# Kernel optimization log

Hardware: AMD Instinct MI355X
Metric: run time of the kernel (lower is better)

The kernel has to match this reference:

```python
import jax, jax.numpy as jnp
import numpy as np

B, N, DIMS, F_DIMS = 4, 16384, 3, 64


def setup_inputs() -> dict:
    key = jax.random.key(0)
    k1, k2, k3 = jax.random.split(key, 3)
    pc = jax.random.normal(k1, (B, N, DIMS), dtype=jnp.float32)
    feats = jax.random.normal(k2, (B, N, F_DIMS), dtype=jnp.float32)
    # single random permutation shared across the batch (tf.random.shuffle(tf.range(N)))
    perm = jax.random.permutation(k3, N).astype(jnp.int32)
    return {"pc": pc, "feats": feats, "perm": perm}


def reference(pc, feats, perm):
    """Faithful JAX port of RandomSample.call.

    pc:    (B, N, dims)   spatial coords
    feats: (B, N, f_dims) features
    perm:  (N,)           random permutation of range(N)
    """
    n = pc.shape[1]
    m = n // 2  # body hardcodes N // 2 regardless of self.scale
    valid_idx = perm[:m]
    invalid_idx = perm[m:]

    valid_pc = jnp.take(pc, valid_idx, axis=1)        # (B, M, dims)
    valid_feats = jnp.take(feats, valid_idx, axis=1)  # (B, M, f_dims)
    invalid_pc = jnp.take(pc, invalid_idx, axis=1)    # (B, M, dims)

    # brute-force KNN: squared euclidean distance of invalid queries vs valid points
    q2 = jnp.sum(invalid_pc * invalid_pc, axis=-1, keepdims=True)   # (B, M, 1)
    p2 = jnp.sum(valid_pc * valid_pc, axis=-1)[:, None, :]          # (B, 1, M)
    cross = jnp.einsum('bqd,bpd->bqp', invalid_pc, valid_pc)        # (B, M, M)
    d2 = q2 - 2.0 * cross + p2                                      # (B, M, M)

    # K=2 nearest; keep the 2nd neighbour index, as in n_idx = knn(...)[:, :, 1]
    _, knn_idx = jax.lax.top_k(-d2, 2)                              # (B, M, 2)
    n_idx = knn_idx[:, :, 1].astype(jnp.int32)                      # (B, M)

    rnds = perm[None, :]  # (1, N), matches tf.expand_dims(shuffle, 0)
    return valid_pc, valid_feats, n_idx, rnds
```

## Files before the change

### kernel.cpp

```cpp
#include <hip/hip_runtime.h>

#define BB 4
#define NN 16384
#define MM 8192
#define FD 64
#define CHUNK 256
#define QPT 2
#define TPB 256
#define QPB (TPB * QPT)

#define OUT0 0
#define OUT1 98304
#define OUT2 2195456
#define OUT3 2228224

#define CAND_BYTES ((size_t)BB * MM * 16)

struct Partial { double m1, m2; };

__device__ __forceinline__ float sumsq3_rn(float x, float y, float z) {
  return __fadd_rn(__fadd_rn(__fmul_rn(x, x), __fmul_rn(y, y)), __fmul_rn(z, z));
}

__device__ __forceinline__ double mkkey(float d2, int k) {
  return __hiloint2double(__float_as_int(d2), k);
}
#define KEY_INIT __hiloint2double(0x7F800000, 0x7FFFFFFF)

__global__ __launch_bounds__(256) void gather_kernel(
    const float* __restrict__ pc, const float* __restrict__ feats,
    const int* __restrict__ perm, float* __restrict__ out,
    float4* __restrict__ cand) {
  int idx = blockIdx.x * 256 + threadIdx.x;
  const int F4_TOT = BB * MM * FD / 4;
  const int PTS    = BB * MM;
  if (idx < F4_TOT) {
    int f4 = idx & 15;
    int r  = (idx >> 4) & (MM - 1);
    int b  = idx >> 17;
    int vi = perm[r];
    const float4* src = (const float4*)(feats + ((b * NN + vi) << 6));
    float4* dst = (float4*)(out + OUT1) + idx;
    *dst = src[f4];
  } else if (idx < F4_TOT + PTS) {
    int k = idx - F4_TOT;
    int r = k & (MM - 1);
    int b = k >> 13;
    int vi = perm[r];
    const float* src = pc + (b * NN + vi) * 3;
    float px = src[0], py = src[1], pz = src[2];
    float* dst = out + OUT0 + k * 3;
    dst[0] = px; dst[1] = py; dst[2] = pz;
    cand[k] = make_float4(px + px, py + py, pz + pz, sumsq3_rn(px, py, pz));
  } else if (idx < F4_TOT + PTS + NN) {
    int k = idx - F4_TOT - PTS;
    out[OUT3 + k] = (float)perm[k];
  }
}

__global__ __launch_bounds__(256) void knn_kernel(
    const float* __restrict__ pc, const int* __restrict__ perm,
    const float4* __restrict__ cand,
    Partial* __restrict__ part, float* __restrict__ out, int nchunk) {
  #pragma clang fp contract(off)
  int blk = blockIdx.x;
  int c  = blk % nchunk;
  int qb = blk / nchunk;
  int q0 = qb * QPB + threadIdx.x;
  int b  = qb >> 4;

  float qx[QPT], qy[QPT], qz[QPT], q2[QPT];
  double m1[QPT], m2[QPT];
  #pragma unroll
  for (int s = 0; s < QPT; ++s) {
    int q = q0 + s * TPB;
    int j = q & (MM - 1);
    int qi = perm[MM + j];
    const float* qp = pc + (b * NN + qi) * 3;
    qx[s] = qp[0]; qy[s] = qp[1]; qz[s] = qp[2];
    q2[s] = sumsq3_rn(qx[s], qy[s], qz[s]);
    m1[s] = KEY_INIT; m2[s] = KEY_INIT;
  }

  __shared__ float4 tile[CHUNK];

  int span = MM / nchunk;
  int begin = c * span, end = begin + span;

  for (int t0 = begin; t0 < end; t0 += CHUNK) {
    __syncthreads();
    tile[threadIdx.x] = cand[b * MM + t0 + threadIdx.x];
    __syncthreads();
    #pragma unroll 8
    for (int k = 0; k < CHUNK; ++k) {
      float4 t = tile[k];
      int idx = t0 + k;
      #pragma unroll
      for (int s = 0; s < QPT; ++s) {
        float cross2 = __fmaf_rn(qz[s], t.z,
                       __fmaf_rn(qy[s], t.y, __fmul_rn(qx[s], t.x)));
        float d2 = __fadd_rn(__fsub_rn(q2[s], cross2), t.w);
        double key = mkkey(d2, idx);
        m2[s] = fmin(fmax(key, m1[s]), m2[s]);
        m1[s] = fmin(key, m1[s]);
      }
    }
  }

  #pragma unroll
  for (int s = 0; s < QPT; ++s) {
    int q = q0 + s * TPB;
    if (part != nullptr) {
      Partial pr; pr.m1 = m1[s]; pr.m2 = m2[s];
      part[q * nchunk + c] = pr;
    } else {
      out[OUT2 + q] = (float)__double2loint(m2[s]);
    }
  }
}

__global__ __launch_bounds__(256) void knn_merge_kernel(
    const Partial* __restrict__ part, float* __restrict__ out, int nchunk) {
  int q = blockIdx.x * 256 + threadIdx.x;
  double m1 = KEY_INIT, m2 = KEY_INIT;
  for (int c = 0; c < nchunk; ++c) {
    Partial p = part[q * nchunk + c];
    m2 = fmin(fmax(p.m1, m1), m2);
    m1 = fmin(p.m1, m1);
    m2 = fmin(fmax(p.m2, m1), m2);
    m1 = fmin(p.m2, m1);
  }
  out[OUT2 + q] = (float)__double2loint(m2);
}

extern "C" void kernel_launch(void* const* d_in, const int* in_sizes, int n_in,
                              void* d_out, int out_size, void* d_ws, size_t ws_size,
                              hipStream_t stream) {
  const float* pc    = (const float*)d_in[0];
  const float* feats = (const float*)d_in[1];
  const int*   perm  = (const int*)d_in[2];
  float* out = (float*)d_out;

  float4* cand = (float4*)d_ws;
  char*   rest = (char*)d_ws + CAND_BYTES;
  size_t  avail = ws_size > CAND_BYTES ? ws_size - CAND_BYTES : 0;

  gather_kernel<<<2240, 256, 0, stream>>>(pc, feats, perm, out, cand);

  int nchunk = 1;
  if      (avail >= (size_t)BB * MM * 32 * sizeof(Partial)) nchunk = 32;
  else if (avail >= (size_t)BB * MM * 16 * sizeof(Partial)) nchunk = 16;
  else if (avail >= (size_t)BB * MM * 8  * sizeof(Partial)) nchunk = 8;
  else if (avail >= (size_t)BB * MM * 4  * sizeof(Partial)) nchunk = 4;
  else if (avail >= (size_t)BB * MM * 2  * sizeof(Partial)) nchunk = 2;

  int qblocks = BB * MM / QPB;
  if (nchunk > 1) {
    Partial* part = (Partial*)rest;
    knn_kernel<<<qblocks * nchunk, TPB, 0, stream>>>(pc, perm, cand, part, out, nchunk);
    knn_merge_kernel<<<BB * MM / 256, 256, 0, stream>>>(part, out, nchunk);
  } else {
    knn_kernel<<<qblocks, TPB, 0, stream>>>(pc, perm, cand, nullptr, out, 1);
  }
}
```

Before: 75.63 us.

## Prune KNN key updates using a precomputed second-nearest distance bound

Adds a bound kernel that computes, for each query, the second-smallest squared distance over the first 512 candidates. The main KNN loop compares each fp32 distance to this bound and only builds the packed double key and runs the min/max updates when a distance could enter the top-2. This removes most of the double-precision fmin/fmax work per candidate in exchange for an extra small kernel, a per-candidate compare and branch, and possible wave divergence.

```diff
diff --git a/kernel.cpp b/kernel.cpp
--- a/kernel.cpp
+++ b/kernel.cpp
@@ -8,18 +8,25 @@
 #define QPT 2
 #define TPB 256
 #define QPB (TPB * QPT)
+#define NBOUND 512
 
 #define OUT0 0
 #define OUT1 98304
 #define OUT2 2195456
 #define OUT3 2228224
 
-#define CAND_BYTES ((size_t)BB * MM * 16)
+#define CAND_BYTES  ((size_t)BB * MM * 16)
+#define BOUND_BYTES ((size_t)BB * MM * 4)
 
 struct Partial { double m1, m2; };
 
 __device__ __forceinline__ float sumsq3_rn(float x, float y, float z) {
   return __fadd_rn(__fadd_rn(__fmul_rn(x, x), __fmul_rn(y, y)), __fmul_rn(z, z));
+}
+__device__ __forceinline__ float dist2_rn(float qx, float qy, float qz, float q2,
+                                          float4 t) {
+  float cross2 = __fmaf_rn(qz, t.z, __fmaf_rn(qy, t.y, __fmul_rn(qx, t.x)));
+  return __fadd_rn(__fsub_rn(q2, cross2), t.w);
 }
 
 __device__ __forceinline__ double mkkey(float d2, int k) {
@@ -58,9 +65,31 @@
   }
 }
 
+__global__ __launch_bounds__(256) void bound_kernel(
+    const float* __restrict__ pc, const int* __restrict__ perm,
+    const float4* __restrict__ cand, float* __restrict__ bound2) {
+  #pragma clang fp contract(off)
+  int q = blockIdx.x * 256 + threadIdx.x;
+  int b = q >> 13;
+  int j = q & (MM - 1);
+  int qi = perm[MM + j];
+  const float* qp = pc + (b * NN + qi) * 3;
+  float qx = qp[0], qy = qp[1], qz = qp[2];
+  float q2 = sumsq3_rn(qx, qy, qz);
+  float m1 = 3.4e38f, m2 = 3.4e38f;
+  const float4* cb = cand + b * MM;
+  #pragma unroll 8
+  for (int k = 0; k < NBOUND; ++k) {
+    float d2 = dist2_rn(qx, qy, qz, q2, cb[k]);
+    m2 = __builtin_amdgcn_fmed3f(d2, m1, m2);
+    m1 = fminf(d2, m1);
+  }
+  bound2[q] = m2;
+}
+
 __global__ __launch_bounds__(256) void knn_kernel(
     const float* __restrict__ pc, const int* __restrict__ perm,
-    const float4* __restrict__ cand,
+    const float4* __restrict__ cand, const float* __restrict__ bound2,
     Partial* __restrict__ part, float* __restrict__ out, int nchunk) {
   #pragma clang fp contract(off)
   int blk = blockIdx.x;
@@ -69,7 +98,7 @@
   int q0 = qb * QPB + threadIdx.x;
   int b  = qb >> 4;
 
-  float qx[QPT], qy[QPT], qz[QPT], q2[QPT];
+  float qx[QPT], qy[QPT], qz[QPT], q2[QPT], bf[QPT];
   double m1[QPT], m2[QPT];
   #pragma unroll
   for (int s = 0; s < QPT; ++s) {
@@ -79,6 +108,7 @@
     const float* qp = pc + (b * NN + qi) * 3;
     qx[s] = qp[0]; qy[s] = qp[1]; qz[s] = qp[2];
     q2[s] = sumsq3_rn(qx[s], qy[s], qz[s]);
+    bf[s] = bound2[q];
     m1[s] = KEY_INIT; m2[s] = KEY_INIT;
   }
 
@@ -91,18 +121,19 @@
     __syncthreads();
     tile[threadIdx.x] = cand[b * MM + t0 + threadIdx.x];
     __syncthreads();
-    #pragma unroll 8
+    #pragma unroll 4
     for (int k = 0; k < CHUNK; ++k) {
       float4 t = tile[k];
       int idx = t0 + k;
-      #pragma unroll
-      for (int s = 0; s < QPT; ++s) {
-        float cross2 = __fmaf_rn(qz[s], t.z,
-                       __fmaf_rn(qy[s], t.y, __fmul_rn(qx[s], t.x)));
-        float d2 = __fadd_rn(__fsub_rn(q2[s], cross2), t.w);
-        double key = mkkey(d2, idx);
-        m2[s] = fmin(fmax(key, m1[s]), m2[s]);
-        m1[s] = fmin(key, m1[s]);
+      float d2a = dist2_rn(qx[0], qy[0], qz[0], q2[0], t);
+      float d2b = dist2_rn(qx[1], qy[1], qz[1], q2[1], t);
+      if (__builtin_expect((d2a <= bf[0]) | (d2b <= bf[1]), 0)) {
+        double ka = mkkey(d2a, idx);
+        double kb = mkkey(d2b, idx);
+        m2[0] = fmin(fmax(ka, m1[0]), m2[0]);
+        m1[0] = fmin(ka, m1[0]);
+        m2[1] = fmin(fmax(kb, m1[1]), m2[1]);
+        m1[1] = fmin(kb, m1[1]);
       }
     }
   }
@@ -141,11 +172,15 @@
   const int*   perm  = (const int*)d_in[2];
   float* out = (float*)d_out;
 
-  float4* cand = (float4*)d_ws;
-  char*   rest = (char*)d_ws + CAND_BYTES;
-  size_t  avail = ws_size > CAND_BYTES ? ws_size - CAND_BYTES : 0;
+  float4* cand   = (float4*)d_ws;
+  float*  bound2 = (float*)((char*)d_ws + CAND_BYTES);
+  char*   rest   = (char*)d_ws + CAND_BYTES + BOUND_BYTES;
+  size_t  used   = CAND_BYTES + BOUND_BYTES;
+  size_t  avail  = ws_size > used ? ws_size - used : 0;
 
   gather_kernel<<<2240, 256, 0, stream>>>(pc, feats, perm, out, cand);
+
+  bound_kernel<<<BB * MM / 256, 256, 0, stream>>>(pc, perm, cand, bound2);
 
   int nchunk = 1;
   if      (avail >= (size_t)BB * MM * 32 * sizeof(Partial)) nchunk = 32;
@@ -157,9 +192,11 @@
   int qblocks = BB * MM / QPB;
   if (nchunk > 1) {
     Partial* part = (Partial*)rest;
-    knn_kernel<<<qblocks * nchunk, TPB, 0, stream>>>(pc, perm, cand, part, out, nchunk);
+    knn_kernel<<<qblocks * nchunk, TPB, 0, stream>>>(pc, perm, cand, bound2,
+                                                     part, out, nchunk);
     knn_merge_kernel<<<BB * MM / 256, 256, 0, stream>>>(part, out, nchunk);
   } else {
-    knn_kernel<<<qblocks, TPB, 0, stream>>>(pc, perm, cand, nullptr, out, 1);
-  }
-}
+    knn_kernel<<<qblocks, TPB, 0, stream>>>(pc, perm, cand, bound2,
+                                            nullptr, out, 1);
+  }
+}
```

New measurement: 109.7 us. +45.1%, slower.

## Prune brute-force KNN via x-coordinate binning and per-query distance bounds

Applied to the files above, without the earlier changes.

Sorts candidate points and queries into 128 bins by x coordinate using histogram, prefix-sum and scatter kernels. A bound kernel computes each query's 2nd-nearest distance over the first 1024 candidates. Each KNN block then scans only the sorted candidate range whose x lies within that bound of its queries. This cuts the full M×M distance scan but adds several small kernels, atomics and a memset, and tie-breaking on equal distances depends on the stored original indices. The META_BYTES macro has an unbalanced parenthesis but is never used, and the bins assume coordinates roughly within ±6.

```diff
diff --git a/kernel.cpp b/kernel.cpp
--- a/kernel.cpp
+++ b/kernel.cpp
@@ -8,24 +8,45 @@
 #define QPT 2
 #define TPB 256
 #define QPB (TPB * QPT)
+#define NBOUND 1024
+#define BINS 128
 
 #define OUT0 0
 #define OUT1 98304
 #define OUT2 2195456
 #define OUT3 2228224
 
+#define CAND_OFF   0
 #define CAND_BYTES ((size_t)BB * MM * 16)
+#define SCAND_OFF  (CAND_OFF + CAND_BYTES)
+#define BOUND_OFF  (SCAND_OFF + CAND_BYTES)
+#define BOUND_BYTES ((size_t)BB * MM * 4)
+#define SKIDX_OFF  (BOUND_OFF + BOUND_BYTES)
+#define SQID_OFF   (SKIDX_OFF + BOUND_BYTES)
+#define META_OFF   (SQID_OFF + BOUND_BYTES)
+#define META_BYTES ((size_t)16384
+#define FIXED_BYTES (META_OFF + 16384)
 
 struct Partial { double m1, m2; };
 
 __device__ __forceinline__ float sumsq3_rn(float x, float y, float z) {
   return __fadd_rn(__fadd_rn(__fmul_rn(x, x), __fmul_rn(y, y)), __fmul_rn(z, z));
 }
-
+__device__ __forceinline__ float dist2_rn(float qx, float qy, float qz, float q2,
+                                          float4 t) {
+  float cross2 = __fmaf_rn(qz, t.z, __fmaf_rn(qy, t.y, __fmul_rn(qx, t.x)));
+  return __fadd_rn(__fsub_rn(q2, cross2), t.w);
+}
 __device__ __forceinline__ double mkkey(float d2, int k) {
   return __hiloint2double(__float_as_int(d2), k);
 }
 #define KEY_INIT __hiloint2double(0x7F800000, 0x7FFFFFFF)
+
+__device__ __forceinline__ int bin128(float v2x) {
+  float f = floorf((v2x + 12.0f) * (BINS / 24.0f));
+  f = fmaxf(0.0f, fminf((float)(BINS - 1), f));
+  return (int)f;
+}
 
 __global__ __launch_bounds__(256) void gather_kernel(
     const float* __restrict__ pc, const float* __restrict__ feats,
@@ -58,49 +79,168 @@
   }
 }
 
+__global__ __launch_bounds__(256) void hist_kernel(
+    const float* __restrict__ pc, const int* __restrict__ perm,
+    const float4* __restrict__ cand, int* __restrict__ meta) {
+  int idx = blockIdx.x * 256 + threadIdx.x;
+  if (idx < BB * MM) {
+    int b = idx >> 13;
+    atomicAdd(&meta[0 + b * BINS + bin128(cand[idx].x)], 1);
+  } else if (idx < 2 * BB * MM) {
+    int qid = idx - BB * MM;
+    int b = qid >> 13, j = qid & (MM - 1);
+    int qi = perm[MM + j];
+    float qx = pc[(b * NN + qi) * 3];
+    atomicAdd(&meta[512 + b * BINS + bin128(qx + qx)], 1);
+  }
+}
+
+__global__ void prefix_kernel(int* __restrict__ meta) {
+  int t = threadIdx.x;
+  if (t < 4) {
+    const int* h = meta + 0 + t * BINS;
+    int* o = meta + 2048 + t * 129;
+    int acc = 0;
+    for (int i = 0; i < BINS; ++i) { o[i] = acc; acc += h[i]; }
+    o[BINS] = acc;
+  } else if (t < 8) {
+    int b = t - 4;
+    const int* h = meta + 512 + b * BINS;
+    int* o = meta + 2564 + b * 129;
+    int acc = 0;
+    for (int i = 0; i < BINS; ++i) { o[i] = acc; acc += h[i]; }
+    o[BINS] = acc;
+  }
+}
+
+__global__ __launch_bounds__(256) void scatter_kernel(
+    const float* __restrict__ pc, const int* __restrict__ perm,
+    const float4* __restrict__ cand, int* __restrict__ meta,
+    float4* __restrict__ scand, int* __restrict__ skidx,
+    int* __restrict__ sqid) {
+  int idx = blockIdx.x * 256 + threadIdx.x;
+  if (idx < BB * MM) {
+    int b = idx >> 13;
+    float4 cv = cand[idx];
+    int bin = bin128(cv.x);
+    int pos = meta[2048 + b * 129 + bin] + atomicAdd(&meta[1024 + b * BINS + bin], 1);
+    int g = (b << 13) + pos;
+    scand[g] = cv;
+    skidx[g] = idx & (MM - 1);
+  } else if (idx < 2 * BB * MM) {
+    int qid = idx - BB * MM;
+    int b = qid >> 13, j = qid & (MM - 1);
+    int qi = perm[MM + j];
+    float qx = pc[(b * NN + qi) * 3];
+    int bin = bin128(qx + qx);
+    int pos = meta[2564 + b * 129 + bin] + atomicAdd(&meta[1536 + b * BINS + bin], 1);
+    sqid[(b << 13) + pos] = j;
+  }
+}
+
+__global__ __launch_bounds__(256) void bound_kernel(
+    const float* __restrict__ pc, const int* __restrict__ perm,
+    const float4* __restrict__ cand, float* __restrict__ bound2) {
+  #pragma clang fp contract(off)
+  int gid = blockIdx.x * 256 + threadIdx.x;
+  int q = gid >> 3, t = gid & 7;
+  int b = q >> 13, j = q & (MM - 1);
+  int qi = perm[MM + j];
+  const float* qp = pc + (b * NN + qi) * 3;
+  float qx = qp[0], qy = qp[1], qz = qp[2];
+  float q2 = sumsq3_rn(qx, qy, qz);
+  float m1 = 3.4e38f, m2 = 3.4e38f;
+  const float4* cb = cand + (b << 13) + t * (NBOUND / 8);
+  #pragma unroll 4
+  for (int i = 0; i < NBOUND / 8; ++i) {
+    float d2 = dist2_rn(qx, qy, qz, q2, cb[i]);
+    m2 = __builtin_amdgcn_fmed3f(d2, m1, m2);
+    m1 = fminf(d2, m1);
+  }
+  #pragma unroll
+  for (int mask = 1; mask < 8; mask <<= 1) {
+    float o1 = __shfl_xor(m1, mask);
+    float o2 = __shfl_xor(m2, mask);
+    float n1 = fminf(m1, o1);
+    float n2 = fminf(fmaxf(m1, o1), fminf(m2, o2));
+    m1 = n1; m2 = n2;
+  }
+  if (t == 0) bound2[q] = m2;
+}
+
 __global__ __launch_bounds__(256) void knn_kernel(
     const float* __restrict__ pc, const int* __restrict__ perm,
-    const float4* __restrict__ cand,
+    const float4* __restrict__ scand, const int* __restrict__ skidx,
+    const int* __restrict__ sqid, const float* __restrict__ bound2,
+    const int* __restrict__ meta,
     Partial* __restrict__ part, float* __restrict__ out, int nchunk) {
   #pragma clang fp contract(off)
-  int blk = blockIdx.x;
-  int c  = blk % nchunk;
-  int qb = blk / nchunk;
-  int q0 = qb * QPB + threadIdx.x;
+  int c  = blockIdx.x % nchunk;
+  int qb = blockIdx.x / nchunk;
   int b  = qb >> 4;
+  int bbase = b << 13;
+  int tid = threadIdx.x;
 
   float qx[QPT], qy[QPT], qz[QPT], q2[QPT];
-  double m1[QPT], m2[QPT];
+  int qorig[QPT];
+  float myLo = 3.4e38f, myHi = -3.4e38f;
   #pragma unroll
   for (int s = 0; s < QPT; ++s) {
-    int q = q0 + s * TPB;
-    int j = q & (MM - 1);
+    int slot = (qb & 15) * QPB + tid + s * TPB;
+    int j = sqid[bbase + slot];
+    qorig[s] = bbase + j;
     int qi = perm[MM + j];
     const float* qp = pc + (b * NN + qi) * 3;
     qx[s] = qp[0]; qy[s] = qp[1]; qz[s] = qp[2];
     q2[s] = sumsq3_rn(qx[s], qy[s], qz[s]);
-    m1[s] = KEY_INIT; m2[s] = KEY_INIT;
-  }
+    float bf = bound2[bbase + j];
+    float r2 = 2.0f * sqrtf(bf + 1e-3f) * 1.0001f;
+    myLo = fminf(myLo, (qx[s] + qx[s]) - r2);
+    myHi = fmaxf(myHi, (qx[s] + qx[s]) + r2);
+  }
+
+  __shared__ float rlo[256], rhi[256];
+  rlo[tid] = myLo; rhi[tid] = myHi;
+  __syncthreads();
+  for (int s2 = 128; s2 > 0; s2 >>= 1) {
+    if (tid < s2) {
+      rlo[tid] = fminf(rlo[tid], rlo[tid + s2]);
+      rhi[tid] = fmaxf(rhi[tid], rhi[tid + s2]);
+    }
+    __syncthreads();
+  }
+  float wlo = rlo[0], whi = rhi[0];
+
+  const int* koff = meta + 2048 + b * 129;
+  int blo = bin128(wlo), bhi = bin128(whi);
+  int plo = bbase + koff[blo];
+  int phi = bbase + koff[bhi + 1];
+  int len = phi - plo;
+  int chunklen = (len + nchunk - 1) / nchunk;
+  int start = plo + c * chunklen;
+  int end = min(start + chunklen, phi);
+
+  double m1[QPT] = {KEY_INIT, KEY_INIT};
+  double m2[QPT] = {KEY_INIT, KEY_INIT};
 
   __shared__ float4 tile[CHUNK];
-
-  int span = MM / nchunk;
-  int begin = c * span, end = begin + span;
-
-  for (int t0 = begin; t0 < end; t0 += CHUNK) {
+  __shared__ int   tidxs[CHUNK];
+
+  for (int t0 = start; t0 < end; t0 += CHUNK) {
     __syncthreads();
-    tile[threadIdx.x] = cand[b * MM + t0 + threadIdx.x];
+    int pos = min(t0 + tid, phi - 1);
+    tile[tid]  = scand[pos];
+    tidxs[tid] = skidx[pos];
     __syncthreads();
-    #pragma unroll 8
-    for (int k = 0; k < CHUNK; ++k) {
+    int kmax = min(CHUNK, end - t0);
+    #pragma unroll 4
+    for (int k = 0; k < kmax; ++k) {
       float4 t = tile[k];
-      int idx = t0 + k;
+      int ki = tidxs[k];
       #pragma unroll
       for (int s = 0; s < QPT; ++s) {
-        float cross2 = __fmaf_rn(qz[s], t.z,
-                       __fmaf_rn(qy[s], t.y, __fmul_rn(qx[s], t.x)));
-        float d2 = __fadd_rn(__fsub_rn(q2[s], cross2), t.w);
-        double key = mkkey(d2, idx);
+        float d2 = dist2_rn(qx[s], qy[s], qz[s], q2[s], t);
+        double key = mkkey(d2, ki);
         m2[s] = fmin(fmax(key, m1[s]), m2[s]);
         m1[s] = fmin(key, m1[s]);
       }
@@ -109,12 +249,11 @@
 
   #pragma unroll
   for (int s = 0; s < QPT; ++s) {
-    int q = q0 + s * TPB;
     if (part != nullptr) {
       Partial pr; pr.m1 = m1[s]; pr.m2 = m2[s];
-      part[q * nchunk + c] = pr;
+      part[qorig[s] * nchunk + c] = pr;
     } else {
-      out[OUT2 + q] = (float)__double2loint(m2[s]);
+      out[OUT2 + qorig[s]] = (float)__double2loint(m2[s]);
     }
   }
 }
@@ -141,11 +280,23 @@
   const int*   perm  = (const int*)d_in[2];
   float* out = (float*)d_out;
 
-  float4* cand = (float4*)d_ws;
-  char*   rest = (char*)d_ws + CAND_BYTES;
-  size_t  avail = ws_size > CAND_BYTES ? ws_size - CAND_BYTES : 0;
+  char* ws = (char*)d_ws;
+  float4* cand   = (float4*)(ws + CAND_OFF);
+  float4* scand  = (float4*)(ws + SCAND_OFF);
+  float*  bound2 = (float*)(ws + BOUND_OFF);
+  int*    skidx  = (int*)(ws + SKIDX_OFF);
+  int*    sqid   = (int*)(ws + SQID_OFF);
+  int*    meta   = (int*)(ws + META_OFF);
+  char*   rest   = ws + FIXED_BYTES;
+  size_t  avail  = ws_size > FIXED_BYTES ? ws_size - FIXED_BYTES : 0;
+
+  hipMemsetAsync(meta, 0, 2048 * sizeof(int), stream);
 
   gather_kernel<<<2240, 256, 0, stream>>>(pc, feats, perm, out, cand);
+  hist_kernel<<<256, 256, 0, stream>>>(pc, perm, cand, meta);
+  prefix_kernel<<<1, 256, 0, stream>>>(meta);
+  scatter_kernel<<<256, 256, 0, stream>>>(pc, perm, cand, meta, scand, skidx, sqid);
+  bound_kernel<<<1024, 256, 0, stream>>>(pc, perm, cand, bound2);
 
   int nchunk = 1;
   if      (avail >= (size_t)BB * MM * 32 * sizeof(Partial)) nchunk = 32;
@@ -157,9 +308,11 @@
   int qblocks = BB * MM / QPB;
   if (nchunk > 1) {
     Partial* part = (Partial*)rest;
-    knn_kernel<<<qblocks * nchunk, TPB, 0, stream>>>(pc, perm, cand, part, out, nchunk);
+    knn_kernel<<<qblocks * nchunk, TPB, 0, stream>>>(pc, perm, scand, skidx, sqid,
+                                                     bound2, meta, part, out, nchunk);
     knn_merge_kernel<<<BB * MM / 256, 256, 0, stream>>>(part, out, nchunk);
   } else {
-    knn_kernel<<<qblocks, TPB, 0, stream>>>(pc, perm, cand, nullptr, out, 1);
-  }
-}
+    knn_kernel<<<qblocks, TPB, 0, stream>>>(pc, perm, scand, skidx, sqid,
+                                            bound2, meta, nullptr, out, 1);
+  }
+}
```

Measured after the change: 194.6 us. 2.57x slower.

## Split KNN into float value scan, chunk merge, and index recovery pass

Applied to the files above, without the earlier changes.

The main scan now tracks only the two smallest float distances per query with fmed3/fmin. It drops the packed double keys that carried the index, which cuts the inner loop to cheap 32-bit ops. A merge kernel finds which chunks hold the top two values, and a recovery kernel rescans only those chunks per query with wavefront-parallel double-key reduction to recover the exact index and tie-breaking. This adds two kernel launches and extra workspace, and the fallback nchunk is now fixed at 8 even if the workspace is smaller.

```diff
diff --git a/kernel.cpp b/kernel.cpp
--- a/kernel.cpp
+++ b/kernel.cpp
@@ -5,23 +5,28 @@
 #define MM 8192
 #define FD 64
 #define CHUNK 256
-#define QPT 2
 #define TPB 256
-#define QPB (TPB * QPT)
+#define QPB 512
 
 #define OUT0 0
 #define OUT1 98304
 #define OUT2 2195456
 #define OUT3 2228224
 
+#define CAND_OFF   0
 #define CAND_BYTES ((size_t)BB * MM * 16)
-
-struct Partial { double m1, m2; };
+#define CPAIR_OFF  (CAND_OFF + CAND_BYTES)
+#define CPAIR_BYTES ((size_t)BB * MM * 8)
+#define PART_OFF   (CPAIR_OFF + CPAIR_BYTES)
 
 __device__ __forceinline__ float sumsq3_rn(float x, float y, float z) {
   return __fadd_rn(__fadd_rn(__fmul_rn(x, x), __fmul_rn(y, y)), __fmul_rn(z, z));
 }
-
+__device__ __forceinline__ float dist2_rn(float qx, float qy, float qz, float q2,
+                                          float4 t) {
+  float cross2 = __fmaf_rn(qz, t.z, __fmaf_rn(qy, t.y, __fmul_rn(qx, t.x)));
+  return __fadd_rn(__fsub_rn(q2, cross2), t.w);
+}
 __device__ __forceinline__ double mkkey(float d2, int k) {
   return __hiloint2double(__float_as_int(d2), k);
 }
@@ -58,28 +63,25 @@
   }
 }
 
-__global__ __launch_bounds__(256) void knn_kernel(
+__global__ __launch_bounds__(256) void knn_val_kernel(
     const float* __restrict__ pc, const int* __restrict__ perm,
-    const float4* __restrict__ cand,
-    Partial* __restrict__ part, float* __restrict__ out, int nchunk) {
+    const float4* __restrict__ cand, float2* __restrict__ part, int nchunk) {
   #pragma clang fp contract(off)
-  int blk = blockIdx.x;
-  int c  = blk % nchunk;
-  int qb = blk / nchunk;
+  int c  = blockIdx.x % nchunk;
+  int qb = blockIdx.x / nchunk;
   int q0 = qb * QPB + threadIdx.x;
   int b  = qb >> 4;
 
-  float qx[QPT], qy[QPT], qz[QPT], q2[QPT];
-  double m1[QPT], m2[QPT];
+  float qx[2], qy[2], qz[2], q2[2], m1[2], m2[2];
   #pragma unroll
-  for (int s = 0; s < QPT; ++s) {
+  for (int s = 0; s < 2; ++s) {
     int q = q0 + s * TPB;
     int j = q & (MM - 1);
     int qi = perm[MM + j];
     const float* qp = pc + (b * NN + qi) * 3;
     qx[s] = qp[0]; qy[s] = qp[1]; qz[s] = qp[2];
     q2[s] = sumsq3_rn(qx[s], qy[s], qz[s]);
-    m1[s] = KEY_INIT; m2[s] = KEY_INIT;
+    m1[s] = 3.4e38f; m2[s] = 3.4e38f;
   }
 
   __shared__ float4 tile[CHUNK];
@@ -94,43 +96,77 @@
     #pragma unroll 8
     for (int k = 0; k < CHUNK; ++k) {
       float4 t = tile[k];
-      int idx = t0 + k;
       #pragma unroll
-      for (int s = 0; s < QPT; ++s) {
-        float cross2 = __fmaf_rn(qz[s], t.z,
-                       __fmaf_rn(qy[s], t.y, __fmul_rn(qx[s], t.x)));
-        float d2 = __fadd_rn(__fsub_rn(q2[s], cross2), t.w);
-        double key = mkkey(d2, idx);
-        m2[s] = fmin(fmax(key, m1[s]), m2[s]);
-        m1[s] = fmin(key, m1[s]);
+      for (int s = 0; s < 2; ++s) {
+        float d2 = dist2_rn(qx[s], qy[s], qz[s], q2[s], t);
+        m2[s] = __builtin_amdgcn_fmed3f(d2, m1[s], m2[s]);
+        m1[s] = fminf(d2, m1[s]);
       }
     }
   }
 
   #pragma unroll
-  for (int s = 0; s < QPT; ++s) {
+  for (int s = 0; s < 2; ++s) {
     int q = q0 + s * TPB;
-    if (part != nullptr) {
-      Partial pr; pr.m1 = m1[s]; pr.m2 = m2[s];
-      part[q * nchunk + c] = pr;
-    } else {
-      out[OUT2 + q] = (float)__double2loint(m2[s]);
-    }
+    part[q * nchunk + c] = make_float2(m1[s], m2[s]);
   }
 }
 
-__global__ __launch_bounds__(256) void knn_merge_kernel(
-    const Partial* __restrict__ part, float* __restrict__ out, int nchunk) {
+__global__ __launch_bounds__(256) void merge_kernel(
+    const float2* __restrict__ part, int2* __restrict__ cpair, int nchunk) {
   int q = blockIdx.x * 256 + threadIdx.x;
+  double k1 = KEY_INIT, k2 = KEY_INIT;
+  for (int c = 0; c < nchunk; ++c) {
+    float2 p = part[q * nchunk + c];
+    double a = mkkey(p.x, c);
+    double d = mkkey(p.y, c);
+    k2 = fmin(fmax(a, k1), k2);
+    k1 = fmin(a, k1);
+    k2 = fmin(fmax(d, k1), k2);
+    k1 = fmin(d, k1);
+  }
+  cpair[q] = make_int2(__double2loint(k1), __double2loint(k2));
+}
+
+__global__ __launch_bounds__(256) void recover_kernel(
+    const float* __restrict__ pc, const int* __restrict__ perm,
+    const float4* __restrict__ cand, const int2* __restrict__ cpair,
+    float* __restrict__ out, int nchunk) {
+  #pragma clang fp contract(off)
+  int wid = threadIdx.x >> 6, lane = threadIdx.x & 63;
+  int q = blockIdx.x * 4 + wid;
+  int b = q >> 13, j = q & (MM - 1);
+  int qi = perm[MM + j];
+  const float* qp = pc + (b * NN + qi) * 3;
+  float qx = qp[0], qy = qp[1], qz = qp[2];
+  float q2 = sumsq3_rn(qx, qy, qz);
+  int2 cp = cpair[q];
+  int clen = MM / nchunk;
+  const float4* cb = cand + (b << 13);
+
   double m1 = KEY_INIT, m2 = KEY_INIT;
-  for (int c = 0; c < nchunk; ++c) {
-    Partial p = part[q * nchunk + c];
-    m2 = fmin(fmax(p.m1, m1), m2);
-    m1 = fmin(p.m1, m1);
-    m2 = fmin(fmax(p.m2, m1), m2);
-    m1 = fmin(p.m2, m1);
+  #pragma unroll
+  for (int pass = 0; pass < 2; ++pass) {
+    int c = pass == 0 ? cp.x : cp.y;
+    if (pass == 1 && cp.y == cp.x) break;
+    int base = c * clen;
+    for (int i = lane; i < clen; i += 64) {
+      float4 t = cb[base + i];
+      float d2 = dist2_rn(qx, qy, qz, q2, t);
+      double key = mkkey(d2, base + i);
+      m2 = fmin(fmax(key, m1), m2);
+      m1 = fmin(key, m1);
+    }
   }
-  out[OUT2 + q] = (float)__double2loint(m2);
+  #pragma unroll
+  for (int mask = 1; mask < 64; mask <<= 1) {
+    double o1 = __shfl_xor(m1, mask);
+    double o2 = __shfl_xor(m2, mask);
+    double n1 = fmin(m1, o1);
+    double n2 = fmin(fmax(m1, o1), fmin(m2, o2));
+    m1 = n1; m2 = n2;
+  }
+  if (lane == 0) out[OUT2 + q] = (float)__double2loint(m2);
 }
 
 extern "C" void kernel_launch(void* const* d_in, const int* in_sizes, int n_in,
@@ -141,25 +177,19 @@
   const int*   perm  = (const int*)d_in[2];
   float* out = (float*)d_out;
 
-  float4* cand = (float4*)d_ws;
-  char*   rest = (char*)d_ws + CAND_BYTES;
-  size_t  avail = ws_size > CAND_BYTES ? ws_size - CAND_BYTES : 0;
+  char* ws = (char*)d_ws;
+  float4* cand  = (float4*)(ws + CAND_OFF);
+  int2*   cpair = (int2*)(ws + CPAIR_OFF);
+  float2* part  = (float2*)(ws + PART_OFF);
+  size_t  avail = ws_size > PART_OFF ? ws_size - PART_OFF : 0;
 
   gather_kernel<<<2240, 256, 0, stream>>>(pc, feats, perm, out, cand);
 
-  int nchunk = 1;
-  if      (avail >= (size_t)BB * MM * 32 * sizeof(Partial)) nchunk = 32;
-  else if (avail >= (size_t)BB * MM * 16 * sizeof(Partial)) nchunk = 16;
-  else if (avail >= (size_t)BB * MM * 8  * sizeof(Partial)) nchunk = 8;
-  else if (avail >= (size_t)BB * MM * 4  * sizeof(Partial)) nchunk = 4;
-  else if (avail >= (size_t)BB * MM * 2  * sizeof(Partial)) nchunk = 2;
+  int nchunk = 8;
+  if      (avail >= (size_t)BB * MM * 32 * sizeof(float2)) nchunk = 32;
+  else if (avail >= (size_t)BB * MM * 16 * sizeof(float2)) nchunk = 16;
 
-  int qblocks = BB * MM / QPB;
-  if (nchunk > 1) {
-    Partial* part = (Partial*)rest;
-    knn_kernel<<<qblocks * nchunk, TPB, 0, stream>>>(pc, perm, cand, part, out, nchunk);
-    knn_merge_kernel<<<BB * MM / 256, 256, 0, stream>>>(part, out, nchunk);
-  } else {
-    knn_kernel<<<qblocks, TPB, 0, stream>>>(pc, perm, cand, nullptr, out, 1);
-  }
+  knn_val_kernel<<<64 * nchunk, TPB, 0, stream>>>(pc, perm, cand, part, nchunk);
+  merge_kernel<<<BB * MM / 256, 256, 0, stream>>>(part, cpair, nchunk);
+  recover_kernel<<<BB * MM / 4, 256, 0, stream>>>(pc, perm, cand, cpair, out, nchunk);
 }
```

After: 77.38 us. 1.02x slower.
